# Optimization experiments

Measured on AMD Instinct MI355X. Metric: run time of the kernel, lower is better.

## Reference

```python
import jax, jax.numpy as jnp
import numpy as np

EPS = 1e-5
N_NODES = 100000
N_EDGES = 1600000
IN_F, HID_F, OUT_F = 128, 128, 64


def setup_inputs() -> dict:
    key = jax.random.key(0)
    ks = jax.random.split(key, 8)
    def xavier(k, fan_in, fan_out):
        lim = float(np.sqrt(6.0 / (fan_in + fan_out)))
        return jax.random.uniform(k, (fan_in, fan_out), jnp.float32, -lim, lim)
    return {
        "features": jax.random.normal(ks[0], (N_NODES, IN_F), jnp.float32),
        "src": jax.random.randint(ks[1], (N_EDGES,), 0, N_NODES, jnp.int64 if jax.config.jax_enable_x64 else jnp.int32),
        "dst": jax.random.randint(ks[2], (N_EDGES,), 0, N_NODES, jnp.int64 if jax.config.jax_enable_x64 else jnp.int32),
        "W_self1": xavier(ks[3], IN_F, HID_F),
        "W_neigh1": xavier(ks[4], IN_F, HID_F),
        "b1": jnp.zeros((HID_F,), jnp.float32),
        "gamma1": jnp.ones((HID_F,), jnp.float32),
        "beta1": jnp.zeros((HID_F,), jnp.float32),
        "W_self2": xavier(ks[5], HID_F, OUT_F),
        "W_neigh2": xavier(ks[6], HID_F, OUT_F),
        "b2": jnp.zeros((OUT_F,), jnp.float32),
        "gamma2": jnp.ones((OUT_F,), jnp.float32),
        "beta2": jnp.zeros((OUT_F,), jnp.float32),
    }


def _sage_conv(h, src, dst, W_self, W_neigh, b, n_nodes):
    # mean aggregation of source-node features onto destination nodes
    agg = jax.ops.segment_sum(h[src], dst, num_segments=n_nodes)   # [N, d]
    deg = jax.ops.segment_sum(jnp.ones_like(dst, dtype=h.dtype), dst, num_segments=n_nodes)
    h_neigh = agg / jnp.maximum(deg, 1.0)[:, None]                  # zero-degree -> 0
    return h @ W_self + h_neigh @ W_neigh + b


def _batchnorm(h, gamma, beta):
    # training-mode BatchNorm1d: batch stats over node dim, biased variance
    mu = jnp.mean(h, axis=0)
    var = jnp.mean(jnp.square(h - mu), axis=0)
    return (h - mu) * jax.lax.rsqrt(var + EPS) * gamma + beta


def reference(features, src, dst, W_self1, W_neigh1, b1, gamma1, beta1,
              W_self2, W_neigh2, b2, gamma2, beta2):
    n = features.shape[0]
    h = _sage_conv(features, src, dst, W_self1, W_neigh1, b1, n)
    h = jax.nn.relu(_batchnorm(h, gamma1, beta1))
    h = _sage_conv(h, src, dst, W_self2, W_neigh2, b2, n)
    return _batchnorm(h, gamma2, beta2)
```

## Files before the change

### kernel.cpp

```cpp
#include <hip/hip_runtime.h>

#define EPS_BN 1e-5f
#define BINSHIFT 9
#define BINW 512
#define P_EPB 8192
#define LDS_CAP 10240
#define NREP 32

typedef __attribute__((ext_vector_type(8))) short short8;
typedef __attribute__((ext_vector_type(4))) float f32x4;

__device__ __forceinline__ unsigned short f2bf(float x) {
    unsigned int u = __float_as_uint(x);
    u += 0x7fffu + ((u >> 16) & 1u);
    return (unsigned short)(u >> 16);
}
__device__ __forceinline__ float bf2f(unsigned short h) {
    return __uint_as_float(((unsigned int)h) << 16);
}
__device__ __forceinline__ float bflo(unsigned u) { return __uint_as_float(u << 16); }
__device__ __forceinline__ float bfhi(unsigned u) { return __uint_as_float(u & 0xffff0000u); }

__device__ __forceinline__ void scan512(int* a, int t) {
    for (int off = 1; off < 512; off <<= 1) {
        int v = (t >= off) ? a[t - off] : 0;
        __syncthreads();
        a[t] += v;
        __syncthreads();
    }
}
__device__ __forceinline__ void scan256(int* a, int t) {
    for (int off = 1; off < 256; off <<= 1) {
        int v = (t >= off) ? a[t - off] : 0;
        __syncthreads();
        a[t] += v;
        __syncthreads();
    }
}

__global__ __launch_bounds__(256) void prep_kernel(
    const float* __restrict__ Ws1, const float* __restrict__ Wn1,
    const float* __restrict__ Ws2, const float* __restrict__ Wn2,
    unsigned short* __restrict__ W1f, unsigned short* __restrict__ W2f,
    const int* __restrict__ dst, int* __restrict__ counts, int E, int NB, int wB) {
    int tid = threadIdx.x;
    if (blockIdx.x < wB) {
        int i = blockIdx.x * 256 + tid;
        if (i < 128 * 256) {
            int j = i & 7, L = (i >> 3) & 63, c = (i >> 9) & 15, kk = i >> 13;
            int k = kk * 32 + (L >> 4) * 8 + j;
            int col = c * 16 + (L & 15);
            float v = (col < 128) ? Ws1[k * 128 + col] : Wn1[k * 128 + (col - 128)];
            W1f[i] = f2bf(v);
        } else {
            int idx = i - 128 * 256;
            if (idx < 128 * 128) {
                int j = idx & 7, L = (idx >> 3) & 63, c = (idx >> 9) & 7, kk = idx >> 12;
                int k = kk * 32 + (L >> 4) * 8 + j;
                int col = c * 16 + (L & 15);
                float v = (col < 64) ? Ws2[k * 64 + col] : Wn2[k * 64 + (col - 64)];
                W2f[idx] = f2bf(v);
            }
        }
    } else {
        __shared__ int hist[512];
        int blk = blockIdx.x - wB;
        int e0 = blk * P_EPB, e1 = min(e0 + P_EPB, E);
        for (int b = tid; b < 512; b += 256) hist[b] = 0;
        __syncthreads();
        for (int e = e0 + tid; e < e1; e += 256) atomicAdd(&hist[dst[e] >> BINSHIFT], 1);
        __syncthreads();
        for (int b = tid; b < NB; b += 256) counts[blk * NB + b] = hist[b];
    }
}

__global__ __launch_bounds__(256) void p2a(const int* __restrict__ counts,
                                           int* __restrict__ segrel,
                                           int* __restrict__ tot, int NB, int NBLK) {
    __shared__ int s[256];
    int b = blockIdx.x, t = threadIdx.x;
    int v = (t < NBLK) ? counts[t * NB + b] : 0;
    s[t] = v;
    __syncthreads();
    scan256(s, t);
    if (t < NBLK) segrel[t * NB + b] = s[t] - v;
    if (t == 255) tot[b] = s[255];
}

__global__ __launch_bounds__(512) void p3_scatter(const int* __restrict__ src,
                                                  const int* __restrict__ dst,
                                                  const int* __restrict__ segrel,
                                                  const int* __restrict__ tot,
                                                  unsigned* __restrict__ epack,
                                                  int E, int NB) {
    __shared__ unsigned lp[P_EPB];
    __shared__ int hist[512];
    __shared__ int sBase[513];
    __shared__ int cursor[512];
    __shared__ int bbase[512];
    int t = threadIdx.x;
    int blk = blockIdx.x;
    int e0 = blk * P_EPB, e1 = min(e0 + P_EPB, E), m = e1 - e0;
    int tv = (t < NB) ? tot[t] : 0;
    bbase[t] = tv;
    __syncthreads();
    scan512(bbase, t);
    bbase[t] -= tv;
    hist[t] = 0;
    __syncthreads();
    for (int e = e0 + t; e < e1; e += 512) atomicAdd(&hist[dst[e] >> BINSHIFT], 1);
    __syncthreads();
    int h = hist[t];
    scan512(hist, t);
    int excl = hist[t] - h;
    sBase[t] = excl;
    cursor[t] = excl;
    if (t == 0) sBase[512] = m;
    __syncthreads();
    for (int e = e0 + t; e < e1; e += 512) {
        int d = dst[e];
        int pos = atomicAdd(&cursor[d >> BINSHIFT], 1);
        lp[pos] = ((unsigned)src[e] << BINSHIFT) | ((unsigned)d & (BINW - 1));
    }
    __syncthreads();
    for (int i = t; i < m; i += 512) {
        int lo = 0, hi = NB;
        while (hi - lo > 1) {
            int mid = (lo + hi) >> 1;
            if (sBase[mid] <= i) lo = mid; else hi = mid;
        }
        epack[bbase[lo] + segrel[blk * NB + lo] + (i - sBase[lo])] = lp[i];
    }
}

__global__ __launch_bounds__(512) void p4_csr(const unsigned* __restrict__ epack,
                                              const int* __restrict__ tot,
                                              int* __restrict__ row_start,
                                              int* __restrict__ cntg,
                                              float* __restrict__ inv_deg,
                                              int* __restrict__ csr_src, int N, int NB) {
    __shared__ int ncnt[512];
    __shared__ int cursor[512];
    __shared__ int bb[512];
    __shared__ int lsrc[LDS_CAP];
    int t = threadIdx.x;
    int b = blockIdx.x;
    int tv = (t < NB) ? tot[t] : 0;
    bb[t] = tv;
    __syncthreads();
    scan512(bb, t);
    int e1 = bb[b];
    int e0 = bb[b] - tot[b];
    int m = e1 - e0;
    int nbase = b << BINSHIFT;
    int nn = min(N - nbase, BINW);
    ncnt[t] = 0;
    __syncthreads();
    for (int i = e0 + t; i < e1; i += 512)
        atomicAdd(&ncnt[epack[i] & (BINW - 1)], 1);
    __syncthreads();
    int c = ncnt[t];
    scan512(ncnt, t);
    int excl = ncnt[t] - c;
    if (t < nn) {
        int node = nbase + t;
        row_start[node] = e0 + excl;
        cntg[node] = c;
        inv_deg[node] = 1.0f / fmaxf((float)c, 1.0f);
    }
    cursor[t] = excl;
    __syncthreads();
    for (int i = e0 + t; i < e1; i += 512) {
        unsigned v = epack[i];
        int pos = atomicAdd(&cursor[v & (BINW - 1)], 1);
        if (pos < LDS_CAP) lsrc[pos] = (int)(v >> BINSHIFT);
    }
    __syncthreads();
    int mm = min(m, LDS_CAP);
    for (int i = t; i < mm; i += 512) csr_src[e0 + i] = lsrc[i];
}

template <int MT, int MSELF, bool SELFBF, bool FUSEBN, bool AFP32>
__global__ __launch_bounds__(256) void gemm_dual(const unsigned short* __restrict__ Ab,
                                                 const float* __restrict__ Af,
                                                 const unsigned short* __restrict__ Wf,
                                                 float* __restrict__ YselfF,
                                                 unsigned short* __restrict__ YselfB,
                                                 unsigned short* __restrict__ Ynb, int N,
                                                 const float* __restrict__ sums,
                                                 const float* __restrict__ gamma,
                                                 const float* __restrict__ beta,
                                                 float invN) {
    constexpr int K = 128;
    constexpr int NCT = MT / 16;
    constexpr int KS = K / 32;
    constexpr int MNB = MT - MSELF;
    __shared__ unsigned short Bl[KS * NCT * 64 * 8];
    __shared__ float ssc[128], ssh[128];

    for (int i = threadIdx.x; i < KS * NCT * 64; i += 256)
        ((short8*)Bl)[i] = ((const short8*)Wf)[i];
    if (FUSEBN && threadIdx.x < 128) {
        int c = threadIdx.x;
        float su = 0.f, sq = 0.f;
        for (int r = 0; r < NREP; r++) {
            su += sums[r * 256 + c];
            sq += sums[r * 256 + 128 + c];
        }
        float mu = su * invN;
        float var = sq * invN - mu * mu;
        float sc = gamma[c] * rsqrtf(var + EPS_BN);
        ssc[c] = sc;
        ssh[c] = beta[c] - mu * sc;
    }
    __syncthreads();

    int wv = threadIdx.x >> 6, lane = threadIdx.x & 63;
    int row0 = blockIdx.x * 128 + wv * 32;
    int m = lane & 15, quad = lane >> 4;

    short8 afrag[2][KS];
#pragma unroll
    for (int t = 0; t < 2; t++) {
        int arow = row0 + t * 16 + m;
        if (arow >= N) arow = N - 1;
#pragma unroll
        for (int kk = 0; kk < KS; kk++) {
            short8 raw;
            if (AFP32) {
                const float* ap = Af + (size_t)arow * K + quad * 8 + kk * 32;
                f32x4 a = *(const f32x4*)ap;
                f32x4 b = *(const f32x4*)(ap + 4);
#pragma unroll
                for (int j = 0; j < 4; j++) {
                    raw[j] = (short)f2bf(a[j]);
                    raw[4 + j] = (short)f2bf(b[j]);
                }
            } else {
                raw = *(const short8*)(Ab + (size_t)arow * K + quad * 8 + kk * 32);
            }
            if (FUSEBN) {
#pragma unroll
                for (int j = 0; j < 8; j++) {
                    int c = kk * 32 + quad * 8 + j;
                    float f = bf2f((unsigned short)raw[j]) * ssc[c] + ssh[c];
                    raw[j] = (short)f2bf(fmaxf(f, 0.f));
                }
            }
            afrag[t][kk] = raw;
        }
    }

    f32x4 acc[2][NCT];
#pragma unroll
    for (int t = 0; t < 2; t++)
        for (int c = 0; c < NCT; c++)
            for (int j = 0; j < 4; j++) acc[t][c][j] = 0.f;

#pragma unroll
    for (int kk = 0; kk < KS; kk++) {
#pragma unroll
        for (int c = 0; c < NCT; c++) {
            short8 bfrag = *(const short8*)&Bl[((kk * NCT + c) * 64 + lane) * 8];
#pragma unroll
            for (int t = 0; t < 2; t++)
                acc[t][c] = __builtin_amdgcn_mfma_f32_16x16x32_bf16(afrag[t][kk], bfrag,
                                                                    acc[t][c], 0, 0, 0);
        }
    }

#pragma unroll
    for (int t = 0; t < 2; t++) {
#pragma unroll
        for (int c = 0; c < NCT; c++) {
            int colg = c * 16 + m;
#pragma unroll
            for (int r = 0; r < 4; r++) {
                int row = row0 + t * 16 + quad * 4 + r;
                if (row < N) {
                    float v = acc[t][c][r];
                    if (colg < MSELF) {
                        if (SELFBF)
                            YselfB[(size_t)row * MSELF + colg] = f2bf(v);
                        else
                            YselfF[(size_t)row * MSELF + colg] = v;
                    } else {
                        Ynb[(size_t)row * MNB + (colg - MSELF)] = f2bf(v);
                    }
                }
            }
        }
    }
}

__global__ __launch_bounds__(256) void agg_row128(const unsigned int* __restrict__ Sb,
                                                  const unsigned int* __restrict__ T,
                                                  const int* __restrict__ row_start,
                                                  const int* __restrict__ cnt,
                                                  const float* __restrict__ inv_deg,
                                                  const int* __restrict__ csr_src,
                                                  const float* __restrict__ bias,
                                                  unsigned int* __restrict__ Out,
                                                  float* __restrict__ sums,
                                                  int N, int totalWaves) {
    int wv = threadIdx.x >> 6, lane = threadIdx.x & 63;
    int c = lane * 2;
    float bs0 = bias[c], bs1 = bias[c + 1];
    float S0 = 0.f, S1 = 0.f, Q0 = 0.f, Q1 = 0.f;

    int n = blockIdx.x * 4 + wv;
    int pStart = 0, pEc = 0, pIv = 0;
    float pInv = 0.f;
    if (n < N) {
        pStart = row_start[n];
        pEc = cnt[n];
        pInv = inv_deg[n];
        if (pEc > 0) pIv = csr_src[pStart + min(lane, min(pEc, 64) - 1)];
    }
    for (; n < N; n += totalWaves) {
        int start = pStart, ec = pEc, iv = pIv;
        float inv = pInv;
        unsigned su = Sb[(size_t)n * 64 + lane];
        int n2 = n + totalWaves;
        if (n2 < N) {
            pStart = row_start[n2];
            pEc = cnt[n2];
            pInv = inv_deg[n2];
            if (pEc > 0) pIv = csr_src[pStart + min(lane, min(pEc, 64) - 1)];
        }
        float a0 = 0.f, a1 = 0.f;
        for (int base = 0; base < ec; base += 64) {
            int ecc = min(ec - base, 64);
            if (base) iv = csr_src[start + base + min(lane, ecc - 1)];
            int e = 0;
            for (; e + 16 <= ecc; e += 16) {
                unsigned u[16];
#pragma unroll
                for (int j = 0; j < 16; j++) {
                    int s = __builtin_amdgcn_readlane(iv, e + j);
                    u[j] = T[(size_t)s * 64 + lane];
                }
#pragma unroll
                for (int j = 0; j < 16; j++) {
                    a0 += bflo(u[j]);
                    a1 += bfhi(u[j]);
                }
            }
            if (e + 8 <= ecc) {
                unsigned u[8];
#pragma unroll
                for (int j = 0; j < 8; j++) {
                    int s = __builtin_amdgcn_readlane(iv, e + j);
                    u[j] = T[(size_t)s * 64 + lane];
                }
#pragma unroll
                for (int j = 0; j < 8; j++) {
                    a0 += bflo(u[j]);
                    a1 += bfhi(u[j]);
                }
                e += 8;
            }
            if (e < ecc) {
                int r = ecc - e;
                unsigned u[8];
#pragma unroll
                for (int j = 0; j < 8; j++) {
                    int s = __builtin_amdgcn_readlane(iv, min(e + j, ecc - 1));
                    u[j] = T[(size_t)s * 64 + lane];
                }
#pragma unroll
                for (int j = 0; j < 8; j++) {
                    if (j < r) {
                        a0 += bflo(u[j]);
                        a1 += bfhi(u[j]);
                    }
                }
            }
        }
        float h0 = bflo(su) + a0 * inv + bs0;
        float h1 = bfhi(su) + a1 * inv + bs1;
        Out[(size_t)n * 64 + lane] = (unsigned)f2bf(h0) | ((unsigned)f2bf(h1) << 16);
        S0 += h0; Q0 += h0 * h0;
        S1 += h1; Q1 += h1 * h1;
    }
    __shared__ float ls[256];
    ls[threadIdx.x] = 0.f;
    __syncthreads();
    atomicAdd(&ls[c], S0);
    atomicAdd(&ls[c + 1], S1);
    atomicAdd(&ls[128 + c], Q0);
    atomicAdd(&ls[129 + c], Q1);
    __syncthreads();
    float* dstS = sums + (size_t)(blockIdx.x & (NREP - 1)) * 256;
    atomicAdd(&dstS[threadIdx.x], ls[threadIdx.x]);
}

__global__ __launch_bounds__(256) void agg_row64(const unsigned int* __restrict__ T,
                                                 const int* __restrict__ row_start,
                                                 const int* __restrict__ cnt,
                                                 const float* __restrict__ inv_deg,
                                                 const int* __restrict__ csr_src,
                                                 const float* __restrict__ bias,
                                                 float* Self, float* __restrict__ sums,
                                                 int N, int totalWaves) {
    int wv = threadIdx.x >> 6, lane = threadIdx.x & 63;
    int g = lane >> 5, h = lane & 31;
    int c = h * 2;
    float bs0 = bias[c], bs1 = bias[c + 1];
    float S0 = 0.f, S1 = 0.f, Q0 = 0.f, Q1 = 0.f;

    int n = blockIdx.x * 4 + wv;
    int pStart = 0, pEc = 0, pIv = 0;
    if (n < N) {
        pStart = row_start[n];
        pEc = cnt[n];
        if (pEc > 0) pIv = csr_src[pStart + min(lane, min(pEc, 64) - 1)];
    }
    for (; n < N; n += totalWaves) {
        int start = pStart, ec = pEc, iv = pIv;
        float inv = inv_deg[n];
        int n2 = n + totalWaves;
        if (n2 < N) {
            pStart = row_start[n2];
            pEc = cnt[n2];
            if (pEc > 0) pIv = csr_src[pStart + min(lane, min(pEc, 64) - 1)];
        }
        float a0 = 0.f, a1 = 0.f;
        for (int base = 0; base < ec; base += 64) {
            int ecc = min(ec - base, 64);
            if (base) iv = csr_src[start + base + min(lane, ecc - 1)];
            int e = 0;
            for (; e + 8 <= ecc; e += 8) {
                unsigned u[4];
#pragma unroll
                for (int j = 0; j < 4; j++) {
                    int s0 = __builtin_amdgcn_readlane(iv, e + 2 * j);
                    int s1 = __builtin_amdgcn_readlane(iv, e + 2 * j + 1);
                    int sg = g ? s1 : s0;
                    u[j] = T[(size_t)sg * 32 + h];
                }
#pragma unroll
                for (int j = 0; j < 4; j++) {
                    a0 += bflo(u[j]);
                    a1 += bfhi(u[j]);
                }
            }
            if (e < ecc) {
                int r = ecc - e;
                unsigned u[4];
#pragma unroll
                for (int j = 0; j < 4; j++) {
                    int s0 = __builtin_amdgcn_readlane(iv, min(e + 2 * j, ecc - 1));
                    int s1 = __builtin_amdgcn_readlane(iv, min(e + 2 * j + 1, ecc - 1));
                    int sg = g ? s1 : s0;
                    u[j] = T[(size_t)sg * 32 + h];
                }
#pragma unroll
                for (int j = 0; j < 4; j++) {
                    bool ok = (2 * j + g) < r;
                    a0 += ok ? bflo(u[j]) : 0.f;
                    a1 += ok ? bfhi(u[j]) : 0.f;
                }
            }
        }
        a0 += __shfl_xor(a0, 32);
        a1 += __shfl_xor(a1, 32);
        if (g == 0) {
            size_t off = (size_t)n * 64 + c;
            float h0 = Self[off] + a0 * inv + bs0;
            float h1 = Self[off + 1] + a1 * inv + bs1;
            Self[off] = h0;
            Self[off + 1] = h1;
            S0 += h0; Q0 += h0 * h0;
            S1 += h1; Q1 += h1 * h1;
        }
    }
    __shared__ float ls[128];
    if (threadIdx.x < 128) ls[threadIdx.x] = 0.f;
    __syncthreads();
    if (g == 0) {
        atomicAdd(&ls[c], S0);
        atomicAdd(&ls[c + 1], S1);
        atomicAdd(&ls[64 + c], Q0);
        atomicAdd(&ls[65 + c], Q1);
    }
    __syncthreads();
    if (threadIdx.x < 128) {
        float* dstS = sums + (size_t)(blockIdx.x & (NREP - 1)) * 128;
        atomicAdd(&dstS[threadIdx.x], ls[threadIdx.x]);
    }
}

__global__ __launch_bounds__(256) void bn_apply_f64(float* H, const float* __restrict__ sums,
                                                    const float* __restrict__ gamma,
                                                    const float* __restrict__ beta,
                                                    int N, float invN) {
    __shared__ float ss[128];
    int tid = threadIdx.x;
    if (tid < 64) {
        float su = 0.f, sq = 0.f;
        for (int r = 0; r < NREP; r++) {
            su += sums[r * 128 + tid];
            sq += sums[r * 128 + 64 + tid];
        }
        float mu = su * invN;
        float var = sq * invN - mu * mu;
        float sc = gamma[tid] * rsqrtf(var + EPS_BN);
        ss[tid] = sc;
        ss[64 + tid] = beta[tid] - mu * sc;
    }
    __syncthreads();
    int total4 = N * 16;
    float4* H4 = (float4*)H;
    for (int i = blockIdx.x * 256 + threadIdx.x; i < total4; i += 256 * gridDim.x) {
        int c0 = (i * 4) & 63;
        float4 v = H4[i];
        float4 sc = *(const float4*)&ss[c0];
        float4 sh = *(const float4*)&ss[64 + c0];
        v.x = v.x * sc.x + sh.x;
        v.y = v.y * sc.y + sh.y;
        v.z = v.z * sc.z + sh.z;
        v.w = v.w * sc.w + sh.w;
        H4[i] = v;
    }
}

extern "C" void kernel_launch(void* const* d_in, const int* in_sizes, int n_in,
                              void* d_out, int out_size, void* d_ws, size_t ws_size,
                              hipStream_t stream) {
    const float* X = (const float*)d_in[0];
    const int* src = (const int*)d_in[1];
    const int* dst = (const int*)d_in[2];
    const float* Wself1 = (const float*)d_in[3];
    const float* Wneigh1 = (const float*)d_in[4];
    const float* b1 = (const float*)d_in[5];
    const float* g1 = (const float*)d_in[6];
    const float* be1 = (const float*)d_in[7];
    const float* Wself2 = (const float*)d_in[8];
    const float* Wneigh2 = (const float*)d_in[9];
    const float* b2 = (const float*)d_in[10];
    const float* g2 = (const float*)d_in[11];
    const float* be2 = (const float*)d_in[12];
    float* out = (float*)d_out;

    const int N = in_sizes[0] / 128;
    const int E = in_sizes[1];
    const int NB = (N + BINW - 1) >> BINSHIFT;
    const int NBLK = (E + P_EPB - 1) / P_EPB;

    char* p = (char*)d_ws;
    auto carve = [&](size_t bytes) {
        char* r = p;
        p += (bytes + 255) & ~(size_t)255;
        return r;
    };
    float* sums1 = (float*)carve((size_t)NREP * 256 * 4);
    float* sums2 = (float*)carve((size_t)NREP * 128 * 4);
    size_t zero_bytes = (size_t)(p - (char*)d_ws);
    int* counts = (int*)carve((size_t)NBLK * NB * 4);
    int* segrel = (int*)carve((size_t)NBLK * NB * 4);
    int* tot = (int*)carve((size_t)NB * 4);
    unsigned* epack = (unsigned*)carve((size_t)E * 4);
    int* csr_src = (int*)carve((size_t)E * 4);
    int* row_start = (int*)carve((size_t)N * 4);
    int* cntg = (int*)carve((size_t)N * 4);
    float* inv_deg = (float*)carve((size_t)N * 4);
    unsigned short* W1f = (unsigned short*)carve(128 * 256 * 2);
    unsigned short* W2f = (unsigned short*)carve(128 * 128 * 2);
    unsigned short* bufS = (unsigned short*)carve((size_t)N * 128 * 2);
    unsigned short* tab = (unsigned short*)carve((size_t)N * 128 * 2);
    unsigned short* h1b = (unsigned short*)carve((size_t)N * 128 * 2);

    hipMemsetAsync(d_ws, 0, zero_bytes, stream);

    const int wB = 192;
    const float invN = 1.0f / (float)N;
    prep_kernel<<<wB + NBLK, 256, 0, stream>>>(Wself1, Wneigh1, Wself2, Wneigh2, W1f, W2f,
                                               dst, counts, E, NB, wB);
    p2a<<<NB, 256, 0, stream>>>(counts, segrel, tot, NB, NBLK);
    p3_scatter<<<NBLK, 512, 0, stream>>>(src, dst, segrel, tot, epack, E, NB);
    p4_csr<<<NB, 512, 0, stream>>>(epack, tot, row_start, cntg, inv_deg, csr_src, N, NB);

    int ggrid = (N + 127) / 128;
    gemm_dual<256, 128, true, false, true><<<ggrid, 256, 0, stream>>>(
        nullptr, X, W1f, nullptr, bufS, tab, N, nullptr, nullptr, nullptr, 0.f);
    agg_row128<<<2048, 256, 0, stream>>>(
        (const unsigned int*)bufS, (const unsigned int*)tab, row_start, cntg, inv_deg,
        csr_src, b1, (unsigned int*)h1b, sums1, N, 8192);

    gemm_dual<128, 64, false, true, false><<<ggrid, 256, 0, stream>>>(
        h1b, nullptr, W2f, out, nullptr, tab, N, sums1, g1, be1, invN);
    agg_row64<<<2048, 256, 0, stream>>>(
        (const unsigned int*)tab, row_start, cntg, inv_deg, csr_src, b2, out, sums2,
        N, 8192);
    bn_apply_f64<<<2048, 256, 0, stream>>>(out, sums2, g2, be2, N, invN);
}
```

Baseline: 354.4 us.

## Quantize neighbor-projection tables to int8 with per-row scales for gather

The GEMM epilogue now stores the neighbor-projected features as int8 with one float scale per row, replacing bf16. Both aggregation kernels gather the int8 pairs plus the row scale and dequantize while accumulating. This halves the bytes moved by the random per-edge gathers, which dominate the aggregation kernels. In exchange it adds a row-max shuffle reduction in the GEMM, an extra scale load per edge, and int8 quantization error that may exceed the accuracy tolerance.

```diff
diff --git a/kernel.cpp b/kernel.cpp
--- a/kernel.cpp
+++ b/kernel.cpp
@@ -20,6 +20,8 @@
 }
 __device__ __forceinline__ float bflo(unsigned u) { return __uint_as_float(u << 16); }
 __device__ __forceinline__ float bfhi(unsigned u) { return __uint_as_float(u & 0xffff0000u); }
+__device__ __forceinline__ float i8lo(unsigned short u) { return (float)(signed char)(u & 0xff); }
+__device__ __forceinline__ float i8hi(unsigned short u) { return (float)(signed char)(u >> 8); }
 
 __device__ __forceinline__ void scan512(int* a, int t) {
     for (int off = 1; off < 512; off <<= 1) {
@@ -186,7 +188,8 @@
                                                  const unsigned short* __restrict__ Wf,
                                                  float* __restrict__ YselfF,
                                                  unsigned short* __restrict__ YselfB,
-                                                 unsigned short* __restrict__ Ynb, int N,
+                                                 signed char* __restrict__ Ynb8,
+                                                 float* __restrict__ scl, int N,
                                                  const float* __restrict__ sums,
                                                  const float* __restrict__ gamma,
                                                  const float* __restrict__ beta,
@@ -195,6 +198,7 @@
     constexpr int NCT = MT / 16;
     constexpr int KS = K / 32;
     constexpr int MNB = MT - MSELF;
+    constexpr int CSELF = MSELF / 16;
     __shared__ unsigned short Bl[KS * NCT * 64 * 8];
     __shared__ float ssc[128], ssh[128];
 
@@ -272,21 +276,36 @@
 #pragma unroll
     for (int t = 0; t < 2; t++) {
 #pragma unroll
-        for (int c = 0; c < NCT; c++) {
+        for (int c = 0; c < CSELF; c++) {
             int colg = c * 16 + m;
 #pragma unroll
             for (int r = 0; r < 4; r++) {
                 int row = row0 + t * 16 + quad * 4 + r;
                 if (row < N) {
                     float v = acc[t][c][r];
-                    if (colg < MSELF) {
-                        if (SELFBF)
-                            YselfB[(size_t)row * MSELF + colg] = f2bf(v);
-                        else
-                            YselfF[(size_t)row * MSELF + colg] = v;
-                    } else {
-                        Ynb[(size_t)row * MNB + (colg - MSELF)] = f2bf(v);
-                    }
+                    if (SELFBF)
+                        YselfB[(size_t)row * MSELF + colg] = f2bf(v);
+                    else
+                        YselfF[(size_t)row * MSELF + colg] = v;
+                }
+            }
+        }
+#pragma unroll
+        for (int r = 0; r < 4; r++) {
+            float mx = 0.f;
+#pragma unroll
+            for (int c = CSELF; c < NCT; c++) mx = fmaxf(mx, fabsf(acc[t][c][r]));
+#pragma unroll
+            for (int off = 1; off < 16; off <<= 1) mx = fmaxf(mx, __shfl_xor(mx, off));
+            int row = row0 + t * 16 + quad * 4 + r;
+            float qs = 127.0f / fmaxf(mx, 1e-30f);
+            if (row < N) {
+                if (m == 0) scl[row] = mx * (1.0f / 127.0f);
+#pragma unroll
+                for (int c = CSELF; c < NCT; c++) {
+                    int colg = c * 16 + m;
+                    int q = __float2int_rn(acc[t][c][r] * qs);
+                    Ynb8[(size_t)row * MNB + (colg - MSELF)] = (signed char)q;
                 }
             }
         }
@@ -294,7 +313,8 @@
 }
 
 __global__ __launch_bounds__(256) void agg_row128(const unsigned int* __restrict__ Sb,
-                                                  const unsigned int* __restrict__ T,
+                                                  const unsigned short* __restrict__ Tq,
+                                                  const float* __restrict__ scl,
                                                   const int* __restrict__ row_start,
                                                   const int* __restrict__ cnt,
                                                   const float* __restrict__ inv_deg,
@@ -334,45 +354,51 @@
             if (base) iv = csr_src[start + base + min(lane, ecc - 1)];
             int e = 0;
             for (; e + 16 <= ecc; e += 16) {
-                unsigned u[16];
+                unsigned short u[16];
+                float sc[16];
 #pragma unroll
                 for (int j = 0; j < 16; j++) {
                     int s = __builtin_amdgcn_readlane(iv, e + j);
-                    u[j] = T[(size_t)s * 64 + lane];
+                    u[j] = Tq[(size_t)s * 64 + lane];
+                    sc[j] = scl[s];
                 }
 #pragma unroll
                 for (int j = 0; j < 16; j++) {
-                    a0 += bflo(u[j]);
-                    a1 += bfhi(u[j]);
+                    a0 += sc[j] * i8lo(u[j]);
+                    a1 += sc[j] * i8hi(u[j]);
                 }
             }
             if (e + 8 <= ecc) {
-                unsigned u[8];
+                unsigned short u[8];
+                float sc[8];
 #pragma unroll
                 for (int j = 0; j < 8; j++) {
                     int s = __builtin_amdgcn_readlane(iv, e + j);
-                    u[j] = T[(size_t)s * 64 + lane];
+                    u[j] = Tq[(size_t)s * 64 + lane];
+                    sc[j] = scl[s];
                 }
 #pragma unroll
                 for (int j = 0; j < 8; j++) {
-                    a0 += bflo(u[j]);
-                    a1 += bfhi(u[j]);
+                    a0 += sc[j] * i8lo(u[j]);
+                    a1 += sc[j] * i8hi(u[j]);
                 }
                 e += 8;
             }
             if (e < ecc) {
                 int r = ecc - e;
-                unsigned u[8];
+                unsigned short u[8];
+                float sc[8];
 #pragma unroll
                 for (int j = 0; j < 8; j++) {
                     int s = __builtin_amdgcn_readlane(iv, min(e + j, ecc - 1));
-                    u[j] = T[(size_t)s * 64 + lane];
+                    u[j] = Tq[(size_t)s * 64 + lane];
+                    sc[j] = scl[s];
                 }
 #pragma unroll
                 for (int j = 0; j < 8; j++) {
                     if (j < r) {
-                        a0 += bflo(u[j]);
-                        a1 += bfhi(u[j]);
+                        a0 += sc[j] * i8lo(u[j]);
+                        a1 += sc[j] * i8hi(u[j]);
                     }
                 }
             }
@@ -395,7 +421,8 @@
     atomicAdd(&dstS[threadIdx.x], ls[threadIdx.x]);
 }
 
-__global__ __launch_bounds__(256) void agg_row64(const unsigned int* __restrict__ T,
+__global__ __launch_bounds__(256) void agg_row64(const unsigned short* __restrict__ Tq,
+                                                 const float* __restrict__ scl,
                                                  const int* __restrict__ row_start,
                                                  const int* __restrict__ cnt,
                                                  const float* __restrict__ inv_deg,
@@ -431,35 +458,39 @@
             if (base) iv = csr_src[start + base + min(lane, ecc - 1)];
             int e = 0;
             for (; e + 8 <= ecc; e += 8) {
-                unsigned u[4];
+                unsigned short u[4];
+                float sc[4];
 #pragma unroll
                 for (int j = 0; j < 4; j++) {
                     int s0 = __builtin_amdgcn_readlane(iv, e + 2 * j);
                     int s1 = __builtin_amdgcn_readlane(iv, e + 2 * j + 1);
                     int sg = g ? s1 : s0;
-                    u[j] = T[(size_t)sg * 32 + h];
+                    u[j] = Tq[(size_t)sg * 32 + h];
+                    sc[j] = scl[sg];
                 }
 #pragma unroll
                 for (int j = 0; j < 4; j++) {
-                    a0 += bflo(u[j]);
-                    a1 += bfhi(u[j]);
+                    a0 += sc[j] * i8lo(u[j]);
+                    a1 += sc[j] * i8hi(u[j]);
                 }
             }
             if (e < ecc) {
                 int r = ecc - e;
-                unsigned u[4];
+                unsigned short u[4];
+                float sc[4];
 #pragma unroll
                 for (int j = 0; j < 4; j++) {
                     int s0 = __builtin_amdgcn_readlane(iv, min(e + 2 * j, ecc - 1));
                     int s1 = __builtin_amdgcn_readlane(iv, min(e + 2 * j + 1, ecc - 1));
                     int sg = g ? s1 : s0;
-                    u[j] = T[(size_t)sg * 32 + h];
+                    u[j] = Tq[(size_t)sg * 32 + h];
+                    sc[j] = scl[sg];
                 }
 #pragma unroll
                 for (int j = 0; j < 4; j++) {
                     bool ok = (2 * j + g) < r;
-                    a0 += ok ? bflo(u[j]) : 0.f;
-                    a1 += ok ? bfhi(u[j]) : 0.f;
+                    a0 += ok ? sc[j] * i8lo(u[j]) : 0.f;
+                    a1 += ok ? sc[j] * i8hi(u[j]) : 0.f;
                 }
             }
         }
@@ -568,7 +599,10 @@
     unsigned short* W1f = (unsigned short*)carve(128 * 256 * 2);
     unsigned short* W2f = (unsigned short*)carve(128 * 128 * 2);
     unsigned short* bufS = (unsigned short*)carve((size_t)N * 128 * 2);
-    unsigned short* tab = (unsigned short*)carve((size_t)N * 128 * 2);
+    signed char* Tq1 = (signed char*)carve((size_t)N * 128);
+    float* scl1 = (float*)carve((size_t)N * 4);
+    signed char* Tq2 = (signed char*)carve((size_t)N * 64);
+    float* scl2 = (float*)carve((size_t)N * 4);
     unsigned short* h1b = (unsigned short*)carve((size_t)N * 128 * 2);
 
     hipMemsetAsync(d_ws, 0, zero_bytes, stream);
@@ -583,15 +617,15 @@
 
     int ggrid = (N + 127) / 128;
     gemm_dual<256, 128, true, false, true><<<ggrid, 256, 0, stream>>>(
-        nullptr, X, W1f, nullptr, bufS, tab, N, nullptr, nullptr, nullptr, 0.f);
+        nullptr, X, W1f, nullptr, bufS, Tq1, scl1, N, nullptr, nullptr, nullptr, 0.f);
     agg_row128<<<2048, 256, 0, stream>>>(
-        (const unsigned int*)bufS, (const unsigned int*)tab, row_start, cntg, inv_deg,
-        csr_src, b1, (unsigned int*)h1b, sums1, N, 8192);
+        (const unsigned int*)bufS, (const unsigned short*)Tq1, scl1, row_start, cntg,
+        inv_deg, csr_src, b1, (unsigned int*)h1b, sums1, N, 8192);
 
     gemm_dual<128, 64, false, true, false><<<ggrid, 256, 0, stream>>>(
-        h1b, nullptr, W2f, out, nullptr, tab, N, sums1, g1, be1, invN);
+        h1b, nullptr, W2f, out, nullptr, Tq2, scl2, N, sums1, g1, be1, invN);
     agg_row64<<<2048, 256, 0, stream>>>(
-        (const unsigned int*)tab, row_start, cntg, inv_deg, csr_src, b2, out, sums2,
-        N, 8192);
+        (const unsigned short*)Tq2, scl2, row_start, cntg, inv_deg, csr_src, b2, out,
+        sums2, N, 8192);
     bn_apply_f64<<<2048, 256, 0, stream>>>(out, sums2, g2, be2, N, invN);
 }
```

Result: no change. 361.3 us (+1.9%).
